# Optimization experiments

Hardware: AMD Instinct MI355X
Metric: run time of the kernel (lower is better)

The kernel has to match this reference:

```python
import jax, jax.numpy as jnp
import numpy as np
from jax import lax

THRESH = 0.8
LENS = 0.4
DECAY = 0.2
LOG_SIG_MIN, LOG_SIG_MAX = -20.0, 2.0
WINS = 15

@jax.custom_vjp
def act_fun(x):
    return (x > THRESH).astype(x.dtype)

def _act_fwd(x):
    return act_fun(x), x

def _act_bwd(x, g):
    return (g * (jnp.abs(x - THRESH) < LENS).astype(g.dtype),)

act_fun.defvjp(_act_fwd, _act_bwd)

B, NIN, HID, NACT = 2048, 512, 1024, 32

def _xavier(key, out_d, in_d):
    lim = jnp.sqrt(6.0 / (in_d + out_d)).astype(jnp.float32)
    return jax.random.uniform(key, (out_d, in_d), jnp.float32, -lim, lim)

def setup_inputs() -> dict:
    key = jax.random.key(0)
    ks = jax.random.split(key, 12)
    inp = {
        'state': jax.random.normal(ks[0], (B, 5, NIN), jnp.float32),
        'w1': _xavier(ks[1], HID, NIN), 'b1': jnp.zeros((HID,), jnp.float32),
        'w2': _xavier(ks[2], HID, NIN), 'b2': jnp.zeros((HID,), jnp.float32),
        'w3': _xavier(ks[3], HID, NIN), 'b3': jnp.zeros((HID,), jnp.float32),
        'wl': _xavier(ks[4], 1, 3), 'bl': jnp.zeros((1,), jnp.float32),
        'w11': _xavier(ks[5], HID, 4 * HID), 'b11': jnp.zeros((HID,), jnp.float32),
        'w12': _xavier(ks[6], HID, HID), 'b12': jnp.zeros((HID,), jnp.float32),
        'w21': _xavier(ks[7], HID, 4 * HID), 'b21': jnp.zeros((HID,), jnp.float32),
        'w22': _xavier(ks[8], HID, HID), 'b22': jnp.zeros((HID,), jnp.float32),
        'wm': _xavier(ks[9], NACT, HID), 'bm': jnp.zeros((NACT,), jnp.float32),
        'ws': _xavier(ks[10], NACT, HID), 'bs': jnp.zeros((NACT,), jnp.float32),
    }
    return inp

def _policy_forward(state, w1, b1, w2, b2, w3, b3, wl, bl,
                    w11, b11, w12, b12, w21, b21, w22, b22, wm, bm, ws, bs):
    batch = state.shape[0]
    hid = w1.shape[0]
    seq = jnp.repeat(state, 3, axis=1)
    mem0 = jnp.zeros((batch, hid, 4), state.dtype)
    sp0 = jnp.zeros((batch, hid, 4), state.dtype)

    def step(carry, x_t):
        mem, spike = carry
        i1 = x_t @ w1.T + b1  # [B, HID]
        i2 = x_t @ w2.T + b2
        i3 = x_t @ w3.T + b3
        inner = jnp.einsum('bck,k->bc', mem[:, :, :3], wl[0]) + bl[0]
        inp_all = jnp.stack([i1, i2, i3, inner], axis=-1)  # [B, HID, 4]
        mem1 = mem * DECAY * (1.0 - spike) + inp_all
        sp1 = act_fun(mem1)
        return (mem1, sp1), sp1

    _, spikes = lax.scan(step, (mem0, sp0), jnp.swapaxes(seq, 0, 1))  # [T,B,HID,4]
    spikes = jnp.transpose(spikes, (1, 0, 2, 3)).reshape(batch, WINS, hid * 4)
    x = jnp.mean(spikes, axis=1)  # [B, 4*HID]

    x1 = jax.nn.relu(x @ w11.T + b11)
    x1 = jax.nn.relu(x1 @ w12.T + b12)
    mean = x1 @ wm.T + bm

    x2 = jax.nn.relu(x @ w21.T + b21)
    x2 = jax.nn.relu(x2 @ w22.T + b22)
    log_std = jnp.clip(x2 @ ws.T + bs, LOG_SIG_MIN, LOG_SIG_MAX)
    return mean, log_std

def reference(state, w1, b1, w2, b2, w3, b3, wl, bl,
              w11, b11, w12, b12, w21, b21, w22, b22, wm, bm, ws, bs):
    return _policy_forward(state, w1, b1, w2, b2, w3, b3, wl, bl,
                           w11, b11, w12, b12, w21, b21, w22, b22, wm, bm, ws, bs)
```

## Files before the change

### kernel.cpp

```cpp
#include <hip/hip_runtime.h>
#include <cstddef>
#include <cstdint>

#define THRESH 0.8f
#define DECAY  0.2f

typedef unsigned short ushort_t;
typedef __attribute__((ext_vector_type(8))) short bf16x8;
typedef __attribute__((ext_vector_type(4))) float f32x4;
typedef __attribute__((ext_vector_type(4))) int i32x4;

__device__ __forceinline__ ushort_t f2bf(float f) {
    union { float f; unsigned u; } v; v.f = f;
    unsigned r = v.u + 0x7FFFu + ((v.u >> 16) & 1u);
    return (ushort_t)(r >> 16);
}
__device__ __forceinline__ float bf2f(ushort_t h) {
    union { unsigned u; float f; } v; v.u = ((unsigned)h) << 16;
    return v.f;
}
__device__ __forceinline__ float blo(unsigned u) {
    union { unsigned x; float f; } v; v.x = u << 16; return v.f;
}
__device__ __forceinline__ float bhi(unsigned u) {
    union { unsigned x; float f; } v; v.x = u & 0xFFFF0000u; return v.f;
}

__device__ __forceinline__ void gload16(const void* g, void* l) {
    __builtin_amdgcn_global_load_lds(
        (const __attribute__((address_space(1))) void*)g,
        (__attribute__((address_space(3))) void*)l,
        16, 0, 0);
}

#define DSREAD(dst, addr, off) \
    asm volatile("ds_read_b128 %0, %1 offset:" #off : "=v"(dst) : "v"(addr))

#define MM(i, j, a, w) \
    acc[i][j] = __builtin_amdgcn_mfma_f32_16x16x32_bf16(a, w, acc[i][j], 0, 0, 0)

__global__ __launch_bounds__(512, 4) void fused_cur_lif(
    const ushort_t* __restrict__ A, const ushort_t* __restrict__ W,
    const float* __restrict__ b123, const float* __restrict__ wl,
    const float* __restrict__ bl, signed char* __restrict__ xb)
{
    __shared__ ushort_t lds[3][11264];

    const int t = threadIdx.x;
    const int bx = blockIdx.x;
    const int by = blockIdx.y;
    const int lane = t & 63;
    const int wv = t >> 6;
    const int wm = (wv >> 2) * 80;
    const int wn = (wv & 3) * 48;
    const int fr = lane & 15;
    const int fq = lane >> 4;
    const int swz16 = (fq ^ ((fr >> 1) & 3)) * 16;

    const unsigned av0 = (unsigned)((wm + fr) * 64 + swz16);
    const unsigned av1 = av0 + 22528;
    const unsigned av2 = av0 + 45056;
    const unsigned bv0 = (unsigned)(10240 + (wn + fr) * 64 + swz16);
    const unsigned bv1 = bv0 + 22528;
    const unsigned bv2 = bv0 + 45056;

    const ushort_t* src0; const ushort_t* src1;
    const ushort_t* src2; const ushort_t* src3;
    int dst0, dst1, dst2, dst3;
    if (wv < 5) {
        const int rl0 = wv * 32 + (lane >> 2);
        const int rl1 = rl0 + 16;
        src0 = A + (size_t)(bx * 160 + rl0) * 1536 + ((lane & 3) ^ ((rl0 >> 1) & 3)) * 8;
        src1 = A + (size_t)(bx * 160 + rl1) * 1536 + ((lane & 3) ^ ((rl1 >> 1) & 3)) * 8;
        src2 = src0; src3 = src1;
        dst0 = rl0 * 32 + (lane & 3) * 8;
        dst1 = rl1 * 32 + (lane & 3) * 8;
        dst2 = dst0; dst3 = dst1;
    } else {
        const int rb = (wv - 5) * 64 + (lane >> 2);
        src0 = W + (size_t)(by * 192 + rb) * 1536 + ((lane & 3) ^ ((rb >> 1) & 3)) * 8;
        src1 = src0 + (size_t)16 * 1536;
        src2 = src0 + (size_t)32 * 1536;
        src3 = src0 + (size_t)48 * 1536;
        dst0 = 5120 + rb * 32 + (lane & 3) * 8;
        dst1 = dst0 + 16 * 32;
        dst2 = dst0 + 32 * 32;
        dst3 = dst0 + 48 * 32;
    }

#define STAGE(tile, sbuf)                                              \
    do {                                                               \
        ushort_t* lb_ = &lds[sbuf][0];                                 \
        if (wv < 5) {                                                  \
            gload16(src0 + (tile) * 32, lb_ + dst0);                   \
            gload16(src1 + (tile) * 32, lb_ + dst1);                   \
        } else {                                                       \
            gload16(src0 + (tile) * 32, lb_ + dst0);                   \
            gload16(src1 + (tile) * 32, lb_ + dst1);                   \
            gload16(src2 + (tile) * 32, lb_ + dst2);                   \
            gload16(src3 + (tile) * 32, lb_ + dst3);                   \
        }                                                              \
    } while (0)

#define COMPUTE(av_, bv_)                                              \
    do {                                                               \
        bf16x8 af0, af1, af2, af3, af4, wf0, wf1, wf2;                 \
        DSREAD(af0, av_, 0);                                           \
        DSREAD(af1, av_, 1024);                                        \
        DSREAD(af2, av_, 2048);                                        \
        DSREAD(af3, av_, 3072);                                        \
        DSREAD(af4, av_, 4096);                                        \
        DSREAD(wf0, bv_, 0);                                           \
        DSREAD(wf1, bv_, 1024);                                        \
        DSREAD(wf2, bv_, 2048);                                        \
        asm volatile("s_waitcnt lgkmcnt(0)" ::: "memory");             \
        __builtin_amdgcn_sched_barrier(0);                             \
        __builtin_amdgcn_s_setprio(1);                                 \
        MM(0, 0, af0, wf0); MM(0, 1, af0, wf1); MM(0, 2, af0, wf2);    \
        MM(1, 0, af1, wf0); MM(1, 1, af1, wf1); MM(1, 2, af1, wf2);    \
        MM(2, 0, af2, wf0); MM(2, 1, af2, wf1); MM(2, 2, af2, wf2);    \
        MM(3, 0, af3, wf0); MM(3, 1, af3, wf1); MM(3, 2, af3, wf2);    \
        MM(4, 0, af4, wf0); MM(4, 1, af4, wf1); MM(4, 2, af4, wf2);    \
        __builtin_amdgcn_s_setprio(0);                                 \
    } while (0)

    f32x4 acc[5][3];
#pragma unroll
    for (int i = 0; i < 5; i++)
#pragma unroll
        for (int j = 0; j < 3; j++) {
            f32x4 z = {0.f, 0.f, 0.f, 0.f};
            acc[i][j] = z;
        }

    STAGE(0, 0);
    STAGE(1, 1);

#pragma unroll
    for (int tt = 0; tt < 46; ++tt) {
        STAGE(tt + 2, (tt + 2) % 3);
        if (wv < 5) asm volatile("s_waitcnt vmcnt(4)" ::: "memory");
        else        asm volatile("s_waitcnt vmcnt(8)" ::: "memory");
        __builtin_amdgcn_s_barrier();
        __builtin_amdgcn_sched_barrier(0);
        const unsigned av_ = (tt % 3 == 0) ? av0 : (tt % 3 == 1) ? av1 : av2;
        const unsigned bv_ = (tt % 3 == 0) ? bv0 : (tt % 3 == 1) ? bv1 : bv2;
        COMPUTE(av_, bv_);
        __builtin_amdgcn_s_barrier();
        __builtin_amdgcn_sched_barrier(0);
    }
    if (wv < 5) asm volatile("s_waitcnt vmcnt(2)" ::: "memory");
    else        asm volatile("s_waitcnt vmcnt(4)" ::: "memory");
    __builtin_amdgcn_s_barrier();
    __builtin_amdgcn_sched_barrier(0);
    COMPUTE(av1, bv1);
    __builtin_amdgcn_s_barrier();
    __builtin_amdgcn_sched_barrier(0);
    asm volatile("s_waitcnt vmcnt(0)" ::: "memory");
    __builtin_amdgcn_s_barrier();
    __builtin_amdgcn_sched_barrier(0);
    COMPUTE(av2, bv2);
#undef STAGE
#undef COMPUTE

    const int ch = by * 64 + (wv & 3) * 16 + fr;
    const float b1c = b123[ch];
    const float b2c = b123[1024 + ch];
    const float b3c = b123[2048 + ch];
    const float wl0 = wl[0], wl1 = wl[1], wl2 = wl[2], bl0 = bl[0];
    const int bbase = bx * 32 + (wv >> 2) * 16 + fq * 4;
#pragma unroll
    for (int r = 0; r < 4; r++) {
        float m0 = 0.f, m1 = 0.f, m2 = 0.f, m3 = 0.f;
        int s0 = 0, s1 = 0, s2 = 0, s3 = 0;
#pragma unroll
        for (int f = 0; f < 5; f++) {
            const float i1 = acc[f][0][r] + b1c;
            const float i2 = acc[f][1][r] + b2c;
            const float i3 = acc[f][2][r] + b3c;
#pragma unroll
            for (int rep = 0; rep < 3; rep++) {
                const float inner = m0 * wl0 + m1 * wl1 + m2 * wl2 + bl0;
                const float n0 = i1 + ((m0 > THRESH) ? 0.f : DECAY * m0);
                const float n1 = i2 + ((m1 > THRESH) ? 0.f : DECAY * m1);
                const float n2 = i3 + ((m2 > THRESH) ? 0.f : DECAY * m2);
                const float n3 = inner + ((m3 > THRESH) ? 0.f : DECAY * m3);
                m0 = n0; m1 = n1; m2 = n2; m3 = n3;
                s0 += (n0 > THRESH); s1 += (n1 > THRESH);
                s2 += (n2 > THRESH); s3 += (n3 > THRESH);
            }
        }
        uchar4 o;
        o.x = (unsigned char)s0; o.y = (unsigned char)s1;
        o.z = (unsigned char)s2; o.w = (unsigned char)s3;
        *(uchar4*)&xb[(size_t)(bbase + r) * 4096 + ch * 4] = o;
    }
}

__global__ __launch_bounds__(256) void mlp1_i8(
    const signed char* __restrict__ A, const signed char* __restrict__ W,
    const float* __restrict__ wsc, const float* __restrict__ bias,
    ushort_t* __restrict__ C)
{
    __shared__ signed char sA[64 * 64];
    __shared__ signed char sW[128 * 64];

    const int t = threadIdx.x;
    const int mBase = blockIdx.x * 64;
    const int nBase = blockIdx.y * 128;

    const int lane = t & 63;
    const int wv = t >> 6;
    const int wn = wv * 32;
    const int fr = lane & 15;
    const int fq = lane >> 4;
    const int fsw = (fq ^ ((fr >> 1) & 3)) * 16;

    const int r0 = t >> 2;
    const int cc = ((t & 3) ^ ((t >> 3) & 3)) * 16;

    i32x4 acc[4][2];
#pragma unroll
    for (int i = 0; i < 4; i++)
#pragma unroll
        for (int j = 0; j < 2; j++) {
            i32x4 z = {0, 0, 0, 0};
            acc[i][j] = z;
        }

    for (int k0 = 0; k0 < 4096; k0 += 64) {
        gload16(&A[(size_t)(mBase + r0) * 4096 + k0 + cc], &sA[t * 16]);
        gload16(&W[(size_t)(nBase + r0) * 4096 + k0 + cc], &sW[t * 16]);
        gload16(&W[(size_t)(nBase + 64 + r0) * 4096 + k0 + cc], &sW[4096 + t * 16]);
        __syncthreads();

        i32x4 af[4], wf[2];
#pragma unroll
        for (int i = 0; i < 4; i++)
            af[i] = *(const i32x4*)&sA[(i * 16 + fr) * 64 + fsw];
#pragma unroll
        for (int j = 0; j < 2; j++)
            wf[j] = *(const i32x4*)&sW[(wn + j * 16 + fr) * 64 + fsw];
#pragma unroll
        for (int i = 0; i < 4; i++)
#pragma unroll
            for (int j = 0; j < 2; j++)
                acc[i][j] = __builtin_amdgcn_mfma_i32_16x16x64_i8(af[i], wf[j], acc[i][j], 0, 0, 0);
        __syncthreads();
    }

#pragma unroll
    for (int j = 0; j < 2; j++) {
        const int col = nBase + wn + j * 16 + fr;
        const float sc = wsc[col];
        const float bv = bias[col];
#pragma unroll
        for (int i = 0; i < 4; i++)
#pragma unroll
            for (int r = 0; r < 4; r++) {
                const int row = mBase + i * 16 + fq * 4 + r;
                const float v = (float)acc[i][j][r] * sc + bv;
                C[(size_t)row * 2048 + col] = f2bf(fmaxf(v, 0.f));
            }
    }
}

__global__ __launch_bounds__(256) void mlp2_bf16(
    const ushort_t* __restrict__ A, const ushort_t* __restrict__ W,
    const float* __restrict__ bias, ushort_t* __restrict__ C,
    int N, int K, int lda, int ldw, int ldc, int aHalfOff)
{
    __shared__ ushort_t sA[64 * 32];
    __shared__ ushort_t sW[128 * 32];

    const int t = threadIdx.x;
    const int mBase = blockIdx.x * 64;
    const int nBase = blockIdx.y * 128;
    const int aOff = (2 * nBase >= N) ? aHalfOff : 0;

    const int lane = t & 63;
    const int wv = t >> 6;
    const int wn = wv * 32;
    const int fr = lane & 15;
    const int fq = lane >> 4;
    const int fsw = (fq ^ ((fr >> 1) & 3)) * 8;

    const int r0 = t >> 2;
    const int cc = ((t & 3) ^ ((t >> 3) & 3)) * 8;

    f32x4 acc[4][2];
#pragma unroll
    for (int i = 0; i < 4; i++)
#pragma unroll
        for (int j = 0; j < 2; j++) {
            f32x4 z = {0.f, 0.f, 0.f, 0.f};
            acc[i][j] = z;
        }

    for (int k0 = 0; k0 < K; k0 += 32) {
        gload16(&A[(size_t)(mBase + r0) * lda + aOff + k0 + cc], &sA[t * 8]);
        gload16(&W[(size_t)(nBase + r0) * ldw + k0 + cc], &sW[t * 8]);
        gload16(&W[(size_t)(nBase + 64 + r0) * ldw + k0 + cc], &sW[2048 + t * 8]);
        __syncthreads();

        bf16x8 af[4], wf[2];
#pragma unroll
        for (int i = 0; i < 4; i++)
            af[i] = *(const bf16x8*)&sA[(i * 16 + fr) * 32 + fsw];
#pragma unroll
        for (int j = 0; j < 2; j++)
            wf[j] = *(const bf16x8*)&sW[(wn + j * 16 + fr) * 32 + fsw];
#pragma unroll
        for (int i = 0; i < 4; i++)
#pragma unroll
            for (int j = 0; j < 2; j++)
                acc[i][j] = __builtin_amdgcn_mfma_f32_16x16x32_bf16(af[i], wf[j], acc[i][j], 0, 0, 0);
        __syncthreads();
    }

#pragma unroll
    for (int j = 0; j < 2; j++) {
        const int col = nBase + wn + j * 16 + fr;
        const float bv = bias[col];
#pragma unroll
        for (int i = 0; i < 4; i++)
#pragma unroll
            for (int r = 0; r < 4; r++) {
                const int row = mBase + i * 16 + fq * 4 + r;
                C[(size_t)row * ldc + col] = f2bf(fmaxf(acc[i][j][r] + bv, 0.f));
            }
    }
}

__device__ __forceinline__ void split_state_perm(const float4* src, ushort4* dst,
                                                 int base, int t) {
#pragma unroll
    for (int p = 0; p < 4; p++) {
        const int i = base * 1024 + p * 256 + t;
        const float4 v = src[i];
        ushort4 h, l;
        h.x = f2bf(v.x); l.x = f2bf(v.x - bf2f(h.x));
        h.y = f2bf(v.y); l.y = f2bf(v.y - bf2f(h.y));
        h.z = f2bf(v.z); l.z = f2bf(v.z - bf2f(h.z));
        h.w = f2bf(v.w); l.w = f2bf(v.w - bf2f(h.w));
        const int s = i >> 7, c4 = i & 127;
        const int b = s / 5, f = s - b * 5;
        const int m = ((b >> 5) * 160) + (((b >> 4) & 1) * 80) + (f << 4) + (b & 15);
        ushort4* row = dst + (size_t)m * 384;
        row[c4] = h; row[128 + c4] = h; row[256 + c4] = l;
    }
}
__device__ __forceinline__ void split_w_perm(const float4* src, ushort4* dst,
                                             int base, int t, int j) {
#pragma unroll
    for (int p = 0; p < 4; p++) {
        const int i = base * 1024 + p * 256 + t;
        const float4 v = src[i];
        ushort4 h, l;
        h.x = f2bf(v.x); l.x = f2bf(v.x - bf2f(h.x));
        h.y = f2bf(v.y); l.y = f2bf(v.y - bf2f(h.y));
        h.z = f2bf(v.z); l.z = f2bf(v.z - bf2f(h.z));
        h.w = f2bf(v.w); l.w = f2bf(v.w - bf2f(h.w));
        const int c = i >> 7, c4 = i & 127;
        const int n = ((c >> 6) * 192) + (((c >> 4) & 3) * 48) + (j << 4) + (c & 15);
        ushort4* row = dst + (size_t)n * 384;
        row[c4] = h; row[128 + c4] = l; row[256 + c4] = h;
    }
}
__device__ __forceinline__ void do_cvt4(const float4* src, ushort4* dst,
                                        int base, int t) {
#pragma unroll
    for (int p = 0; p < 4; p++) {
        const int i = base * 1024 + p * 256 + t;
        const float4 v = src[i];
        ushort4 h;
        h.x = f2bf(v.x); h.y = f2bf(v.y); h.z = f2bf(v.z); h.w = f2bf(v.w);
        dst[i] = h;
    }
}
__device__ __forceinline__ int q8(float x, float inv) {
    int q = (int)rintf(x * inv);
    q = q > 127 ? 127 : (q < -127 ? -127 : q);
    return q & 0xff;
}

__global__ __launch_bounds__(256) void prep_kernel(
    const float* __restrict__ state,
    const float* __restrict__ w1, const float* __restrict__ w2,
    const float* __restrict__ w3,
    const float* __restrict__ w11, const float* __restrict__ w21,
    const float* __restrict__ w12, const float* __restrict__ w22,
    const float* __restrict__ b1, const float* __restrict__ b2,
    const float* __restrict__ b3, const float* __restrict__ b11,
    const float* __restrict__ b21, const float* __restrict__ b12,
    const float* __restrict__ b22,
    ushort_t* __restrict__ Ap, ushort_t* __restrict__ Wp,
    signed char* __restrict__ w1q, float* __restrict__ wsc,
    ushort_t* __restrict__ w2b,
    float* __restrict__ b123, float* __restrict__ bb1, float* __restrict__ bb2)
{
    const int bid = blockIdx.x;
    const int t = threadIdx.x;
    if (bid < 1280) {
        split_state_perm((const float4*)state, (ushort4*)Ap, bid, t);
    } else if (bid < 1408) {
        split_w_perm((const float4*)w1, (ushort4*)Wp, bid - 1280, t, 0);
    } else if (bid < 1536) {
        split_w_perm((const float4*)w2, (ushort4*)Wp, bid - 1408, t, 1);
    } else if (bid < 1664) {
        split_w_perm((const float4*)w3, (ushort4*)Wp, bid - 1536, t, 2);
    } else if (bid < 3712) {
        const int r = bid - 1664;
        const float* src = (r < 1024) ? (w11 + (size_t)r * 4096)
                                      : (w21 + (size_t)(r - 1024) * 4096);
        __shared__ float red4[4];
        float4 v[4];
        float lmax = 0.f;
#pragma unroll
        for (int p = 0; p < 4; p++) {
            v[p] = ((const float4*)src)[t * 4 + p];
            lmax = fmaxf(lmax, fmaxf(fmaxf(fabsf(v[p].x), fabsf(v[p].y)),
                                     fmaxf(fabsf(v[p].z), fabsf(v[p].w))));
        }
#pragma unroll
        for (int d = 1; d < 64; d <<= 1)
            lmax = fmaxf(lmax, __shfl_xor(lmax, d, 64));
        if ((t & 63) == 0) red4[t >> 6] = lmax;
        __syncthreads();
        const float gmax = fmaxf(fmaxf(fmaxf(red4[0], red4[1]),
                                       fmaxf(red4[2], red4[3])), 1e-30f);
        const float inv = 127.0f / gmax;
        int4 o;
        o.x = q8(v[0].x, inv) | (q8(v[0].y, inv) << 8) | (q8(v[0].z, inv) << 16) | (q8(v[0].w, inv) << 24);
        o.y = q8(v[1].x, inv) | (q8(v[1].y, inv) << 8) | (q8(v[1].z, inv) << 16) | (q8(v[1].w, inv) << 24);
        o.z = q8(v[2].x, inv) | (q8(v[2].y, inv) << 8) | (q8(v[2].z, inv) << 16) | (q8(v[2].w, inv) << 24);
        o.w = q8(v[3].x, inv) | (q8(v[3].y, inv) << 8) | (q8(v[3].z, inv) << 16) | (q8(v[3].w, inv) << 24);
        ((int4*)(w1q + (size_t)r * 4096))[t] = o;
        if (t == 0) wsc[r] = gmax / (127.0f * 15.0f);
    } else if (bid < 3968) {
        do_cvt4((const float4*)w12, (ushort4*)w2b, bid - 3712, t);
    } else if (bid < 4224) {
        do_cvt4((const float4*)w22, (ushort4*)(w2b + 1048576), bid - 3968, t);
    } else {
#pragma unroll
        for (int p = 0; p < 4; p++) {
            const int i = p * 256 + t;
            b123[i] = b1[i]; b123[1024 + i] = b2[i]; b123[2048 + i] = b3[i];
            bb1[i] = b11[i]; bb1[1024 + i] = b21[i];
            bb2[i] = b12[i]; bb2[1024 + i] = b22[i];
        }
    }
}

__global__ __launch_bounds__(256) void head_kernel(
    const ushort_t* __restrict__ h, const float* __restrict__ wm,
    const float* __restrict__ bm, const float* __restrict__ ws,
    const float* __restrict__ bs, float* __restrict__ out)
{
    const int t = threadIdx.x;
    const int branch = blockIdx.x >> 8;
    const int n = t & 31;
    const int b = (blockIdx.x & 255) * 8 + (t >> 5);
    const ushort_t* hr = h + (size_t)b * 2048 + branch * 1024;
    const float* wr = (branch ? ws : wm) + (size_t)n * 1024;
    float s = 0.f;
#pragma unroll 4
    for (int k = 0; k < 1024; k += 8) {
        const uint4 hv = *(const uint4*)&hr[k];
        const float4 w0 = *(const float4*)&wr[k];
        const float4 w1 = *(const float4*)&wr[k + 4];
        s += blo(hv.x) * w0.x + bhi(hv.x) * w0.y
           + blo(hv.y) * w0.z + bhi(hv.y) * w0.w
           + blo(hv.z) * w1.x + bhi(hv.z) * w1.y
           + blo(hv.w) * w1.z + bhi(hv.w) * w1.w;
    }
    s += (branch ? bs : bm)[n];
    if (branch) s = fminf(fmaxf(s, -20.f), 2.f);
    out[(size_t)branch * 65536 + (size_t)b * 32 + n] = s;
}

extern "C" void kernel_launch(void* const* d_in, const int* in_sizes, int n_in,
                              void* d_out, int out_size, void* d_ws, size_t ws_size,
                              hipStream_t stream)
{
    const float* state = (const float*)d_in[0];
    const float* w1  = (const float*)d_in[1];  const float* b1  = (const float*)d_in[2];
    const float* w2  = (const float*)d_in[3];  const float* b2  = (const float*)d_in[4];
    const float* w3  = (const float*)d_in[5];  const float* b3  = (const float*)d_in[6];
    const float* wl  = (const float*)d_in[7];  const float* bl  = (const float*)d_in[8];
    const float* w11 = (const float*)d_in[9];  const float* b11 = (const float*)d_in[10];
    const float* w12 = (const float*)d_in[11]; const float* b12 = (const float*)d_in[12];
    const float* w21 = (const float*)d_in[13]; const float* b21 = (const float*)d_in[14];
    const float* w22 = (const float*)d_in[15]; const float* b22 = (const float*)d_in[16];
    const float* wm  = (const float*)d_in[17]; const float* bm  = (const float*)d_in[18];
    const float* ws  = (const float*)d_in[19]; const float* bs  = (const float*)d_in[20];
    float* out = (float*)d_out;

    char* wp = (char*)d_ws;
    ushort_t*    Ap    = (ushort_t*)wp;    wp += (size_t)10240 * 1536 * 2;
    ushort_t*    Wp    = (ushort_t*)wp;    wp += (size_t)3072 * 1536 * 2;
    signed char* xb    = (signed char*)wp; wp += (size_t)2048 * 4096;
    signed char* w1q   = (signed char*)wp; wp += (size_t)2048 * 4096;
    ushort_t*    w2b   = (ushort_t*)wp;    wp += (size_t)2048 * 1024 * 2;
    ushort_t*    h1    = (ushort_t*)wp;    wp += (size_t)2048 * 2048 * 2;
    ushort_t*    h2    = (ushort_t*)wp;    wp += (size_t)2048 * 2048 * 2;
    float*       wsc   = (float*)wp;       wp += 2048 * 4;
    float*       b123  = (float*)wp;       wp += 3072 * 4;
    float*       bb1   = (float*)wp;       wp += 2048 * 4;
    float*       bb2   = (float*)wp;       wp += 2048 * 4;

    prep_kernel<<<4225, 256, 0, stream>>>(
        state, w1, w2, w3, w11, w21, w12, w22,
        b1, b2, b3, b11, b21, b12, b22,
        Ap, Wp, w1q, wsc, w2b, b123, bb1, bb2);

    fused_cur_lif<<<dim3(64, 16), 512, 0, stream>>>(Ap, Wp, b123, wl, bl, xb);

    mlp1_i8<<<dim3(32, 16), 256, 0, stream>>>(xb, w1q, wsc, bb1, h1);

    mlp2_bf16<<<dim3(32, 16), 256, 0, stream>>>(
        h1, w2b, bb2, h2, 2048, 1024, 2048, 1024, 2048, 1024);

    head_kernel<<<512, 256, 0, stream>>>(h2, wm, bm, ws, bs, out);
}
```

Before: 368.4 us.

## Triple-buffer LDS with prefetch pipeline in int8 and bf16 MLP GEMMs

Rewrites both MLP GEMM kernels to use a three-stage LDS ring buffer. Global-to-LDS loads are issued two tiles ahead, and explicit vmcnt waits replace the two __syncthreads per tile. Fragment reads use precomputed LDS offsets, MFMA blocks are wrapped in setprio, and launch bounds request two blocks per CU. The aim is to hide global load latency behind MFMA work, at the cost of more LDS per block and hard-coded trip counts that assume K=4096 and K=1024.

```diff
diff --git a/kernel.cpp b/kernel.cpp
--- a/kernel.cpp
+++ b/kernel.cpp
@@ -197,13 +197,12 @@
     }
 }
 
-__global__ __launch_bounds__(256) void mlp1_i8(
+__global__ __launch_bounds__(256, 2) void mlp1_i8(
     const signed char* __restrict__ A, const signed char* __restrict__ W,
     const float* __restrict__ wsc, const float* __restrict__ bias,
     ushort_t* __restrict__ C)
 {
-    __shared__ signed char sA[64 * 64];
-    __shared__ signed char sW[128 * 64];
+    __shared__ signed char lds[3][12288];
 
     const int t = threadIdx.x;
     const int mBase = blockIdx.x * 64;
@@ -216,8 +215,47 @@
     const int fq = lane >> 4;
     const int fsw = (fq ^ ((fr >> 1) & 3)) * 16;
 
+    const unsigned a0 = (unsigned)(fr * 64 + fsw);
+    const unsigned a1 = a0 + 12288, a2 = a0 + 24576;
+    const unsigned b0 = (unsigned)(4096 + (wn + fr) * 64 + fsw);
+    const unsigned b1 = b0 + 12288, b2 = b0 + 24576;
+
     const int r0 = t >> 2;
-    const int cc = ((t & 3) ^ ((t >> 3) & 3)) * 16;
+    const int cc = ((t & 3) ^ ((r0 >> 1) & 3)) * 16;
+    const signed char* srcA  = A + (size_t)(mBase + r0) * 4096 + cc;
+    const signed char* srcW0 = W + (size_t)(nBase + r0) * 4096 + cc;
+    const signed char* srcW1 = W + (size_t)(nBase + 64 + r0) * 4096 + cc;
+
+#define STAGE1(tile)                                                   \
+    do {                                                               \
+        signed char* lb_ = &lds[(tile) % 3][0];                        \
+        gload16(srcA  + (tile) * 64, lb_ + t * 16);                    \
+        gload16(srcW0 + (tile) * 64, lb_ + 4096 + t * 16);             \
+        gload16(srcW1 + (tile) * 64, lb_ + 8192 + t * 16);             \
+    } while (0)
+
+#define COMPUTE1(av_, bv_)                                             \
+    do {                                                               \
+        i32x4 af0, af1, af2, af3, wf0, wf1;                            \
+        DSREAD(af0, av_, 0);                                           \
+        DSREAD(af1, av_, 1024);                                        \
+        DSREAD(af2, av_, 2048);                                        \
+        DSREAD(af3, av_, 3072);                                        \
+        DSREAD(wf0, bv_, 0);                                           \
+        DSREAD(wf1, bv_, 1024);                                        \
+        asm volatile("s_waitcnt lgkmcnt(0)" ::: "memory");             \
+        __builtin_amdgcn_sched_barrier(0);                             \
+        __builtin_amdgcn_s_setprio(1);                                 \
+        acc[0][0] = __builtin_amdgcn_mfma_i32_16x16x64_i8(af0, wf0, acc[0][0], 0, 0, 0); \
+        acc[0][1] = __builtin_amdgcn_mfma_i32_16x16x64_i8(af0, wf1, acc[0][1], 0, 0, 0); \
+        acc[1][0] = __builtin_amdgcn_mfma_i32_16x16x64_i8(af1, wf0, acc[1][0], 0, 0, 0); \
+        acc[1][1] = __builtin_amdgcn_mfma_i32_16x16x64_i8(af1, wf1, acc[1][1], 0, 0, 0); \
+        acc[2][0] = __builtin_amdgcn_mfma_i32_16x16x64_i8(af2, wf0, acc[2][0], 0, 0, 0); \
+        acc[2][1] = __builtin_amdgcn_mfma_i32_16x16x64_i8(af2, wf1, acc[2][1], 0, 0, 0); \
+        acc[3][0] = __builtin_amdgcn_mfma_i32_16x16x64_i8(af3, wf0, acc[3][0], 0, 0, 0); \
+        acc[3][1] = __builtin_amdgcn_mfma_i32_16x16x64_i8(af3, wf1, acc[3][1], 0, 0, 0); \
+        __builtin_amdgcn_s_setprio(0);                                 \
+    } while (0)
 
     i32x4 acc[4][2];
 #pragma unroll
@@ -228,26 +266,33 @@
             acc[i][j] = z;
         }
 
-    for (int k0 = 0; k0 < 4096; k0 += 64) {
-        gload16(&A[(size_t)(mBase + r0) * 4096 + k0 + cc], &sA[t * 16]);
-        gload16(&W[(size_t)(nBase + r0) * 4096 + k0 + cc], &sW[t * 16]);
-        gload16(&W[(size_t)(nBase + 64 + r0) * 4096 + k0 + cc], &sW[4096 + t * 16]);
-        __syncthreads();
-
-        i32x4 af[4], wf[2];
-#pragma unroll
-        for (int i = 0; i < 4; i++)
-            af[i] = *(const i32x4*)&sA[(i * 16 + fr) * 64 + fsw];
-#pragma unroll
-        for (int j = 0; j < 2; j++)
-            wf[j] = *(const i32x4*)&sW[(wn + j * 16 + fr) * 64 + fsw];
-#pragma unroll
-        for (int i = 0; i < 4; i++)
-#pragma unroll
-            for (int j = 0; j < 2; j++)
-                acc[i][j] = __builtin_amdgcn_mfma_i32_16x16x64_i8(af[i], wf[j], acc[i][j], 0, 0, 0);
-        __syncthreads();
-    }
+    STAGE1(0);
+    STAGE1(1);
+
+#pragma unroll
+    for (int tt = 0; tt < 62; ++tt) {
+        STAGE1(tt + 2);
+        asm volatile("s_waitcnt vmcnt(6)" ::: "memory");
+        __builtin_amdgcn_s_barrier();
+        __builtin_amdgcn_sched_barrier(0);
+        const unsigned av_ = (tt % 3 == 0) ? a0 : (tt % 3 == 1) ? a1 : a2;
+        const unsigned bv_ = (tt % 3 == 0) ? b0 : (tt % 3 == 1) ? b1 : b2;
+        COMPUTE1(av_, bv_);
+        __builtin_amdgcn_s_barrier();
+        __builtin_amdgcn_sched_barrier(0);
+    }
+    asm volatile("s_waitcnt vmcnt(3)" ::: "memory");
+    __builtin_amdgcn_s_barrier();
+    __builtin_amdgcn_sched_barrier(0);
+    COMPUTE1(a2, b2);
+    __builtin_amdgcn_s_barrier();
+    __builtin_amdgcn_sched_barrier(0);
+    asm volatile("s_waitcnt vmcnt(0)" ::: "memory");
+    __builtin_amdgcn_s_barrier();
+    __builtin_amdgcn_sched_barrier(0);
+    COMPUTE1(a0, b0);
+#undef STAGE1
+#undef COMPUTE1
 
 #pragma unroll
     for (int j = 0; j < 2; j++) {
@@ -265,13 +310,12 @@
     }
 }
 
-__global__ __launch_bounds__(256) void mlp2_bf16(
+__global__ __launch_bounds__(256, 2) void mlp2_bf16(
     const ushort_t* __restrict__ A, const ushort_t* __restrict__ W,
     const float* __restrict__ bias, ushort_t* __restrict__ C,
     int N, int K, int lda, int ldw, int ldc, int aHalfOff)
 {
-    __shared__ ushort_t sA[64 * 32];
-    __shared__ ushort_t sW[128 * 32];
+    __shared__ ushort_t lds[3][6144];
 
     const int t = threadIdx.x;
     const int mBase = blockIdx.x * 64;
@@ -283,10 +327,45 @@
     const int wn = wv * 32;
     const int fr = lane & 15;
     const int fq = lane >> 4;
-    const int fsw = (fq ^ ((fr >> 1) & 3)) * 8;
+    const int fsw = (fq ^ ((fr >> 1) & 3)) * 16;
+
+    const unsigned a0 = (unsigned)(fr * 64 + fsw);
+    const unsigned a1 = a0 + 12288, a2 = a0 + 24576;
+    const unsigned b0 = (unsigned)(4096 + (wn + fr) * 64 + fsw);
+    const unsigned b1 = b0 + 12288, b2 = b0 + 24576;
 
     const int r0 = t >> 2;
-    const int cc = ((t & 3) ^ ((t >> 3) & 3)) * 8;
+    const int cc = ((t & 3) ^ ((r0 >> 1) & 3)) * 8;
+    const ushort_t* srcA  = A + (size_t)(mBase + r0) * lda + aOff + cc;
+    const ushort_t* srcW0 = W + (size_t)(nBase + r0) * ldw + cc;
+    const ushort_t* srcW1 = W + (size_t)(nBase + 64 + r0) * ldw + cc;
+
+#define STAGE2(tile)                                                   \
+    do {                                                               \
+        char* lb_ = (char*)&lds[(tile) % 3][0];                        \
+        gload16(srcA  + (tile) * 32, lb_ + t * 16);                    \
+        gload16(srcW0 + (tile) * 32, lb_ + 4096 + t * 16);             \
+        gload16(srcW1 + (tile) * 32, lb_ + 8192 + t * 16);             \
+    } while (0)
+
+#define COMPUTE2(av_, bv_)                                             \
+    do {                                                               \
+        bf16x8 af0, af1, af2, af3, wf0, wf1;                           \
+        DSREAD(af0, av_, 0);                                           \
+        DSREAD(af1, av_, 1024);                                        \
+        DSREAD(af2, av_, 2048);                                        \
+        DSREAD(af3, av_, 3072);                                        \
+        DSREAD(wf0, bv_, 0);                                           \
+        DSREAD(wf1, bv_, 1024);                                        \
+        asm volatile("s_waitcnt lgkmcnt(0)" ::: "memory");             \
+        __builtin_amdgcn_sched_barrier(0);                             \
+        __builtin_amdgcn_s_setprio(1);                                 \
+        MM(0, 0, af0, wf0); MM(0, 1, af0, wf1);                        \
+        MM(1, 0, af1, wf0); MM(1, 1, af1, wf1);                        \
+        MM(2, 0, af2, wf0); MM(2, 1, af2, wf1);                        \
+        MM(3, 0, af3, wf0); MM(3, 1, af3, wf1);                        \
+        __builtin_amdgcn_s_setprio(0);                                 \
+    } while (0)
 
     f32x4 acc[4][2];
 #pragma unroll
@@ -297,26 +376,33 @@
             acc[i][j] = z;
         }
 
-    for (int k0 = 0; k0 < K; k0 += 32) {
-        gload16(&A[(size_t)(mBase + r0) * lda + aOff + k0 + cc], &sA[t * 8]);
-        gload16(&W[(size_t)(nBase + r0) * ldw + k0 + cc], &sW[t * 8]);
-        gload16(&W[(size_t)(nBase + 64 + r0) * ldw + k0 + cc], &sW[2048 + t * 8]);
-        __syncthreads();
-
-        bf16x8 af[4], wf[2];
-#pragma unroll
-        for (int i = 0; i < 4; i++)
-            af[i] = *(const bf16x8*)&sA[(i * 16 + fr) * 32 + fsw];
-#pragma unroll
-        for (int j = 0; j < 2; j++)
-            wf[j] = *(const bf16x8*)&sW[(wn + j * 16 + fr) * 32 + fsw];
-#pragma unroll
-        for (int i = 0; i < 4; i++)
-#pragma unroll
-            for (int j = 0; j < 2; j++)
-                acc[i][j] = __builtin_amdgcn_mfma_f32_16x16x32_bf16(af[i], wf[j], acc[i][j], 0, 0, 0);
-        __syncthreads();
-    }
+    STAGE2(0);
+    STAGE2(1);
+
+#pragma unroll
+    for (int tt = 0; tt < 30; ++tt) {
+        STAGE2(tt + 2);
+        asm volatile("s_waitcnt vmcnt(6)" ::: "memory");
+        __builtin_amdgcn_s_barrier();
+        __builtin_amdgcn_sched_barrier(0);
+        const unsigned av_ = (tt % 3 == 0) ? a0 : (tt % 3 == 1) ? a1 : a2;
+        const unsigned bv_ = (tt % 3 == 0) ? b0 : (tt % 3 == 1) ? b1 : b2;
+        COMPUTE2(av_, bv_);
+        __builtin_amdgcn_s_barrier();
+        __builtin_amdgcn_sched_barrier(0);
+    }
+    asm volatile("s_waitcnt vmcnt(3)" ::: "memory");
+    __builtin_amdgcn_s_barrier();
+    __builtin_amdgcn_sched_barrier(0);
+    COMPUTE2(a0, b0);
+    __builtin_amdgcn_s_barrier();
+    __builtin_amdgcn_sched_barrier(0);
+    asm volatile("s_waitcnt vmcnt(0)" ::: "memory");
+    __builtin_amdgcn_s_barrier();
+    __builtin_amdgcn_sched_barrier(0);
+    COMPUTE2(a1, b1);
+#undef STAGE2
+#undef COMPUTE2
 
 #pragma unroll
     for (int j = 0; j < 2; j++) {
```

New measurement: 353.1 us. 4.2% less time.
